# Performance work log

Hardware: AMD Instinct MI355X
Metric: run time of the kernel (lower is better)

The kernel has to match this reference:

```python
import jax, jax.numpy as jnp
import numpy as np

EPS_F = 1e-12
M, N = 64, 4096  # feature dim m, num nodes n


def setup_inputs() -> dict:
    key = jax.random.key(0)
    k1, k2, k3, k4 = jax.random.split(key, 4)
    # X: (m, n) node features transposed, as in the repo (features.t())
    X = jax.random.normal(k1, (M, N), dtype=jnp.float32)
    # F: (m, m) parameter, xavier_uniform init
    bound = float(np.sqrt(6.0 / (M + M)))
    F = jax.random.uniform(k2, (M, M), minval=-bound, maxval=bound, dtype=jnp.float32)
    # Q_S: (n, n) orthogonal eigenvector matrix of the (symmetric, normalized) adjacency
    A = jax.random.normal(k3, (N, N), dtype=jnp.float32)
    Q_S, _ = jnp.linalg.qr(A)
    Q_S = Q_S.astype(jnp.float32)
    # Lambda_S: (n, 1) eigenvalues of normalized adjacency, inside (-1, 1)
    Lambda_S = jnp.sort(
        jax.random.uniform(k4, (N, 1), minval=-0.95, maxval=0.95, dtype=jnp.float32), axis=0
    )
    gamma = jnp.asarray(0.8, dtype=jnp.float32)
    return {"X": X, "F": F, "Q_S": Q_S, "Lambda_S": Lambda_S, "gamma": gamma}


def reference(X, F, Q_S, Lambda_S, gamma):
    # g(F) = F^T F / (||F^T F||_F + eps)  -- Frobenius-normalized Gram matrix
    FF = F.T @ F                                   # (m, m)
    G_F = FF / (jnp.linalg.norm(FF) + EPS_F)       # (m, m), symmetric PSD, ||.||_F ~ 1
    # spectral decomposition of g(F)
    Lambda_F, Q_F = jnp.linalg.eigh(G_F)           # (m,), (m, m)
    # closed-form equilibrium of Z = gamma * g(F) Z S^T + X in the joint eigenbasis
    D = 1.0 / (1.0 - gamma * Lambda_F[:, None] * Lambda_S.reshape(1, -1))  # (m, n)
    Z = Q_F @ (D * (Q_F.T @ X @ Q_S)) @ Q_S.T      # (m, n)
    return Z
```

## Files before the change

kernel.cpp:

```cpp
#include <hip/hip_runtime.h>
#include <math.h>


typedef short short8 __attribute__((ext_vector_type(8)));
typedef float floatx16 __attribute__((ext_vector_type(16)));

#define KSPLIT 16
#define KCHUNK 256
constexpr int Mdim = 64;
constexpr int Ndim = 4096;
constexpr int SLAB = Mdim * Ndim;

__device__ inline ushort f2bf(float f) {
    uint u = __float_as_uint(f);
    u += 0x7fff + ((u >> 16) & 1);
    return (ushort)(u >> 16);
}
__device__ inline float bf2f(ushort h) { return __uint_as_float(((uint)h) << 16); }

__device__ inline floatx16 mfma_bf16(short8 a, short8 b, floatx16 c) {
    return __builtin_amdgcn_mfma_f32_32x32x16_bf16(a, b, c, 0, 0, 0);
}

struct SharedGemm { ushort Ah[4096], Al[4096], Bh[4096], Bl[4096]; };
struct SharedPrep { float Fraw[64 * 65]; ushort Ph[4096], Pl[4096]; float red[256]; };
union SharedU { SharedGemm g; SharedPrep p; };

__device__ void prep_body(SharedPrep& sp, const float* __restrict__ F, float* __restrict__ Gout) {
    const int t = threadIdx.x;
    const int l = t & 63, w = t >> 6;
    const int tm = w & 1, tn = w >> 1;
    const int am = tm * 32 + (l & 31);
    const int bn = tn * 32 + (l & 31);
    const int lk = l >> 5;

    for (int s = 0; s < 4; ++s) {
        int e = t + 256 * s;
        int r = e >> 4, q = (e & 15) * 4;
        float4 v = *(const float4*)&F[r * 64 + q];
        float fa[4] = {v.x, v.y, v.z, v.w};
        for (int i = 0; i < 4; ++i) sp.Fraw[r * 65 + q + i] = fa[i];
    }
    __syncthreads();
    {
        int c = t >> 2, kbase = (t & 3) * 16;
        ushort hh[16], ll[16];
#pragma unroll
        for (int kk = 0; kk < 16; ++kk) {
            float v = sp.Fraw[(kbase + kk) * 65 + c];
            ushort h = f2bf(v);
            hh[kk] = h;
            ll[kk] = f2bf(v - bf2f(h));
        }
#pragma unroll
        for (int g = 0; g < 2; ++g) {
            int gk = (kbase >> 3) + g;
            int idx = c * 64 + ((gk ^ (c & 7)) * 8);
#pragma unroll
            for (int u = 0; u < 8; ++u) { sp.Ph[idx + u] = hh[8 * g + u]; sp.Pl[idx + u] = ll[8 * g + u]; }
        }
    }
    __syncthreads();
    floatx16 acc;
    for (int i = 0; i < 16; ++i) acc[i] = 0.f;
    for (int s16 = 0; s16 < 4; ++s16) {
        int gk = 2 * s16 + lk;
        int ai = am * 64 + ((gk ^ (am & 7)) * 8);
        int bi = bn * 64 + ((gk ^ (bn & 7)) * 8);
        short8 ah = *(const short8*)&sp.Ph[ai];
        short8 al = *(const short8*)&sp.Pl[ai];
        short8 bh = *(const short8*)&sp.Ph[bi];
        short8 bl = *(const short8*)&sp.Pl[bi];
        acc = mfma_bf16(ah, bh, acc);
        acc = mfma_bf16(al, bh, acc);
        acc = mfma_bf16(ah, bl, acc);
    }
    float ss = 0.f;
    for (int r = 0; r < 16; ++r) ss += acc[r] * acc[r];
    sp.red[t] = ss;
    __syncthreads();
    for (int off = 128; off > 0; off >>= 1) {
        if (t < off) sp.red[t] += sp.red[t + off];
        __syncthreads();
    }
    const float inv = 1.0f / (sqrtf(sp.red[0]) + 1e-12f);
    for (int r = 0; r < 16; ++r) {
        int row = (r & 3) + 8 * (r >> 2) + 4 * lk + tm * 32;
        int col = tn * 32 + (l & 31);
        float v = acc[r] * inv;
        Gout[row * 64 + col] = v;
        ushort h = f2bf(v);
        int idx = row * 64 + (((col >> 3) ^ (row & 7)) * 8 + (col & 7));
        sp.Ph[idx] = h;
        sp.Pl[idx] = f2bf(v - bf2f(h));
    }
    for (int j = 1; j < 5; ++j) {
        __syncthreads();
        floatx16 a2;
        for (int i = 0; i < 16; ++i) a2[i] = 0.f;
        for (int s16 = 0; s16 < 4; ++s16) {
            int gk = 2 * s16 + lk;
            int ai = am * 64 + ((gk ^ (am & 7)) * 8);
            int bi = bn * 64 + ((gk ^ (bn & 7)) * 8);
            short8 ah = *(const short8*)&sp.Ph[ai];
            short8 al = *(const short8*)&sp.Pl[ai];
            short8 bh = *(const short8*)&sp.Ph[bi];
            short8 bl = *(const short8*)&sp.Pl[bi];
            a2 = mfma_bf16(ah, bh, a2);
            a2 = mfma_bf16(al, bh, a2);
            a2 = mfma_bf16(ah, bl, a2);
        }
        __syncthreads();
        for (int r = 0; r < 16; ++r) {
            int row = (r & 3) + 8 * (r >> 2) + 4 * lk + tm * 32;
            int col = tn * 32 + (l & 31);
            float v = a2[r];
            Gout[j * 4096 + row * 64 + col] = v;
            ushort h = f2bf(v);
            int idx = row * 64 + (((col >> 3) ^ (row & 7)) * 8 + (col & 7));
            sp.Ph[idx] = h;
            sp.Pl[idx] = f2bf(v - bf2f(h));
        }
    }
}

template <bool TB, bool DOPREP>
__global__ __launch_bounds__(256, 4) void gemm_kernel(const float* __restrict__ A,
                                                      const float* __restrict__ Bm,
                                                      float* __restrict__ C,
                                                      const float* __restrict__ F,
                                                      float* __restrict__ Gp) {
    __shared__ SharedU sh;
    const int bid = blockIdx.x;
    if (DOPREP) {
        if (bid == 0) { prep_body(sh.p, F, Gp); return; }
    }
    const int b = DOPREP ? bid - 1 : bid;
    const int n0 = (b & 63) * 64;
    const int kb = (b >> 6) * KCHUNK;
    const int t = threadIdx.x;
    const int l = t & 63, w = t >> 6;
    const int tm = w & 1, tn = w >> 1;
    const int am = tm * 32 + (l & 31);
    const int bn = tn * 32 + (l & 31);
    const int lk = l >> 5;
    const int sr = t >> 2, sj = t & 3;
    const int nq = t & 15, kr2 = 2 * (t >> 4);

    floatx16 acc;
    for (int i = 0; i < 16; ++i) acc[i] = 0.f;

    for (int step = 0; step < KCHUNK / 64; ++step) {
        const int k0 = kb + step * 64;
        float4 av[4], bv[4], bva[2], bvb[2];
        for (int s = 0; s < 4; ++s)
            av[s] = *(const float4*)&A[sr * 4096 + k0 + 4 * sj + 16 * s];
        if (TB) {
            for (int s = 0; s < 4; ++s)
                bv[s] = *(const float4*)&Bm[(size_t)(n0 + sr) * 4096 + k0 + 4 * sj + 16 * s];
        } else {
            for (int s = 0; s < 2; ++s) {
                bva[s] = *(const float4*)&Bm[(size_t)(k0 + kr2 + 32 * s) * 4096 + n0 + 4 * nq];
                bvb[s] = *(const float4*)&Bm[(size_t)(k0 + kr2 + 1 + 32 * s) * 4096 + n0 + 4 * nq];
            }
        }
        __syncthreads();
        for (int s = 0; s < 4; ++s) {
            int off = 4 * sj + 16 * s;
            int idx = sr * 64 + (((off >> 3) ^ (sr & 7)) * 8 + (off & 7));
            float fa[4] = {av[s].x, av[s].y, av[s].z, av[s].w};
            ushort4 h4, l4;
            ushort* hp = (ushort*)&h4; ushort* lp = (ushort*)&l4;
            for (int i = 0; i < 4; ++i) {
                ushort h = f2bf(fa[i]);
                hp[i] = h; lp[i] = f2bf(fa[i] - bf2f(h));
            }
            *(ushort4*)&sh.g.Ah[idx] = h4;
            *(ushort4*)&sh.g.Al[idx] = l4;
        }
        if (TB) {
            for (int s = 0; s < 4; ++s) {
                int off = 4 * sj + 16 * s;
                int idx = sr * 64 + (((off >> 3) ^ (sr & 7)) * 8 + (off & 7));
                float fb[4] = {bv[s].x, bv[s].y, bv[s].z, bv[s].w};
                ushort4 h4, l4;
                ushort* hp = (ushort*)&h4; ushort* lp = (ushort*)&l4;
                for (int i = 0; i < 4; ++i) {
                    ushort h = f2bf(fb[i]);
                    hp[i] = h; lp[i] = f2bf(fb[i] - bf2f(h));
                }
                *(ushort4*)&sh.g.Bh[idx] = h4;
                *(ushort4*)&sh.g.Bl[idx] = l4;
            }
        } else {
            for (int s = 0; s < 2; ++s) {
                int k = kr2 + 32 * s;
                float fa[4] = {bva[s].x, bva[s].y, bva[s].z, bva[s].w};
                float fb[4] = {bvb[s].x, bvb[s].y, bvb[s].z, bvb[s].w};
                for (int i = 0; i < 4; ++i) {
                    int n = 4 * nq + i;
                    int idx = n * 64 + (((k >> 3) ^ (n & 7)) * 8 + (k & 7));
                    ushort2 hp2, lp2;
                    hp2.x = f2bf(fa[i]); hp2.y = f2bf(fb[i]);
                    lp2.x = f2bf(fa[i] - bf2f(hp2.x));
                    lp2.y = f2bf(fb[i] - bf2f(hp2.y));
                    *(ushort2*)&sh.g.Bh[idx] = hp2;
                    *(ushort2*)&sh.g.Bl[idx] = lp2;
                }
            }
        }
        __syncthreads();
#pragma unroll
        for (int s16 = 0; s16 < 4; ++s16) {
            int gk = 2 * s16 + lk;
            int ai = am * 64 + ((gk ^ (am & 7)) * 8);
            int bi = bn * 64 + ((gk ^ (bn & 7)) * 8);
            short8 ah = *(const short8*)&sh.g.Ah[ai];
            short8 al = *(const short8*)&sh.g.Al[ai];
            short8 bh = *(const short8*)&sh.g.Bh[bi];
            short8 bl = *(const short8*)&sh.g.Bl[bi];
            acc = mfma_bf16(ah, bh, acc);
            acc = mfma_bf16(al, bh, acc);
            acc = mfma_bf16(ah, bl, acc);
        }
    }
    float* Cslab = C + (size_t)(b >> 6) * SLAB;
    const int colg = n0 + tn * 32 + (l & 31);
#pragma unroll
    for (int r = 0; r < 16; ++r) {
        int row = (r & 3) + 8 * (r >> 2) + 4 * lk + tm * 32;
        Cslab[row * 4096 + colg] = acc[r];
    }
}

__global__ __launch_bounds__(256) void solve_kernel(const float* __restrict__ W,
                                                    const float* __restrict__ Gp,
                                                    const float* __restrict__ lam,
                                                    const float* __restrict__ gammap,
                                                    float* __restrict__ Y) {
    __shared__ float Gs[64][68];
    __shared__ float T[64][17];
    const int t = threadIdx.x;
    const int c0 = blockIdx.x * 16;
    for (int e = t; e < 1024; e += 256) {
        const int r = e >> 4, c = c0 + (e & 15);
        float s = 0.f;
#pragma unroll
        for (int bsl = 0; bsl < KSPLIT; ++bsl) s += W[bsl * SLAB + r * 4096 + c];
        T[r][e & 15] = s;
    }
    const int tx = t & 15;
    const int r4 = (t >> 4) * 4;
    const float a = gammap[0] * lam[c0 + tx];
    float s = a;
    for (int j = 0; j < 5; ++j) {
        __syncthreads();
        for (int e = t; e < 4096; e += 256) Gs[e >> 6][e & 63] = Gp[j * 4096 + e];
        __syncthreads();
        float u0 = 0.f, u1 = 0.f, u2 = 0.f, u3 = 0.f;
#pragma unroll 8
        for (int k = 0; k < 64; ++k) {
            const float tv = T[k][tx];
            const float4 g = *(const float4*)&Gs[k][r4];
            u0 += g.x * tv; u1 += g.y * tv; u2 += g.z * tv; u3 += g.w * tv;
        }
        __syncthreads();
        T[r4 + 0][tx] += s * u0;
        T[r4 + 1][tx] += s * u1;
        T[r4 + 2][tx] += s * u2;
        T[r4 + 3][tx] += s * u3;
        s = s * s;
    }
    __syncthreads();
    for (int e = t; e < 1024; e += 256)
        Y[(e >> 4) * 4096 + c0 + (e & 15)] = T[e >> 4][e & 15];
}

__global__ __launch_bounds__(256) void reduce_kernel(const float* __restrict__ P,
                                                     float* __restrict__ Z) {
    const int i = blockIdx.x * 256 + threadIdx.x;
    float4 a = {0.f, 0.f, 0.f, 0.f};
#pragma unroll
    for (int bsl = 0; bsl < KSPLIT; ++bsl) {
        float4 v = *(const float4*)&P[(size_t)bsl * SLAB + i * 4];
        a.x += v.x; a.y += v.y; a.z += v.z; a.w += v.w;
    }
    *(float4*)&Z[i * 4] = a;
}

extern "C" void kernel_launch(void* const* d_in, const int* in_sizes, int n_in,
                              void* d_out, int out_size, void* d_ws, size_t ws_size,
                              hipStream_t stream) {
    const float* X     = (const float*)d_in[0];
    const float* F     = (const float*)d_in[1];
    const float* Qs    = (const float*)d_in[2];
    const float* lam   = (const float*)d_in[3];
    const float* gamma = (const float*)d_in[4];
    float* Z = (float*)d_out;

    float* P1 = (float*)d_ws;
    float* P2 = P1 + (size_t)KSPLIT * SLAB;
    float* Gp = P2 + (size_t)KSPLIT * SLAB;
    float* Y  = Gp + 5 * 4096;

    gemm_kernel<false, true><<<64 * KSPLIT + 1, 256, 0, stream>>>(X, Qs, P1, F, Gp);
    solve_kernel<<<Ndim / 16, 256, 0, stream>>>(P1, Gp, lam, gamma, Y);
    gemm_kernel<true, false><<<64 * KSPLIT, 256, 0, stream>>>(Y, Qs, P2, nullptr, nullptr);
    reduce_kernel<<<256, 256, 0, stream>>>(P2, Z);
}
```

Baseline: 170.3 us.

## Replace split-K partial slabs with atomic accumulation and halve split factor

The split-K GEMMs now accumulate directly into a single output with float atomicAdd instead of writing per-split slabs that later get summed. This removes the separate reduce kernel and the slab summation in the solve kernel. The split factor drops from 16 to 8 with larger K chunks, and a zero-init kernel is added. It cuts workspace traffic and one launch, at the cost of atomic contention, nondeterministic summation order and fewer blocks.

```diff
diff --git a/kernel.cpp b/kernel.cpp
--- a/kernel.cpp
+++ b/kernel.cpp
@@ -5,11 +5,10 @@
 typedef short short8 __attribute__((ext_vector_type(8)));
 typedef float floatx16 __attribute__((ext_vector_type(16)));
 
-#define KSPLIT 16
-#define KCHUNK 256
+#define KSPLIT 8
+#define KCHUNK 512
 constexpr int Mdim = 64;
 constexpr int Ndim = 4096;
-constexpr int SLAB = Mdim * Ndim;
 
 __device__ inline ushort f2bf(float f) {
     uint u = __float_as_uint(f);
@@ -25,6 +24,13 @@
 struct SharedGemm { ushort Ah[4096], Al[4096], Bh[4096], Bl[4096]; };
 struct SharedPrep { float Fraw[64 * 65]; ushort Ph[4096], Pl[4096]; float red[256]; };
 union SharedU { SharedGemm g; SharedPrep p; };
+
+__global__ __launch_bounds__(256) void init_kernel(float* __restrict__ W, float* __restrict__ Z) {
+    const int i = blockIdx.x * 256 + threadIdx.x;
+    float4 z = {0.f, 0.f, 0.f, 0.f};
+    if (i < 65536) *(float4*)&W[i * 4] = z;
+    else *(float4*)&Z[(i - 65536) * 4] = z;
+}
 
 __device__ void prep_body(SharedPrep& sp, const float* __restrict__ F, float* __restrict__ Gout) {
     const int t = threadIdx.x;
@@ -224,12 +230,11 @@
             acc = mfma_bf16(ah, bl, acc);
         }
     }
-    float* Cslab = C + (size_t)(b >> 6) * SLAB;
     const int colg = n0 + tn * 32 + (l & 31);
 #pragma unroll
     for (int r = 0; r < 16; ++r) {
         int row = (r & 3) + 8 * (r >> 2) + 4 * lk + tm * 32;
-        Cslab[row * 4096 + colg] = acc[r];
+        atomicAdd(&C[row * 4096 + colg], acc[r]);
     }
 }
 
@@ -242,13 +247,8 @@
     __shared__ float T[64][17];
     const int t = threadIdx.x;
     const int c0 = blockIdx.x * 16;
-    for (int e = t; e < 1024; e += 256) {
-        const int r = e >> 4, c = c0 + (e & 15);
-        float s = 0.f;
-#pragma unroll
-        for (int bsl = 0; bsl < KSPLIT; ++bsl) s += W[bsl * SLAB + r * 4096 + c];
-        T[r][e & 15] = s;
-    }
+    for (int e = t; e < 1024; e += 256)
+        T[e >> 4][e & 15] = W[(e >> 4) * 4096 + c0 + (e & 15)];
     const int tx = t & 15;
     const int r4 = (t >> 4) * 4;
     const float a = gammap[0] * lam[c0 + tx];
@@ -274,18 +274,6 @@
     __syncthreads();
     for (int e = t; e < 1024; e += 256)
         Y[(e >> 4) * 4096 + c0 + (e & 15)] = T[e >> 4][e & 15];
-}
-
-__global__ __launch_bounds__(256) void reduce_kernel(const float* __restrict__ P,
-                                                     float* __restrict__ Z) {
-    const int i = blockIdx.x * 256 + threadIdx.x;
-    float4 a = {0.f, 0.f, 0.f, 0.f};
-#pragma unroll
-    for (int bsl = 0; bsl < KSPLIT; ++bsl) {
-        float4 v = *(const float4*)&P[(size_t)bsl * SLAB + i * 4];
-        a.x += v.x; a.y += v.y; a.z += v.z; a.w += v.w;
-    }
-    *(float4*)&Z[i * 4] = a;
 }
 
 extern "C" void kernel_launch(void* const* d_in, const int* in_sizes, int n_in,
@@ -298,13 +286,12 @@
     const float* gamma = (const float*)d_in[4];
     float* Z = (float*)d_out;
 
-    float* P1 = (float*)d_ws;
-    float* P2 = P1 + (size_t)KSPLIT * SLAB;
-    float* Gp = P2 + (size_t)KSPLIT * SLAB;
-    float* Y  = Gp + 5 * 4096;
-
-    gemm_kernel<false, true><<<64 * KSPLIT + 1, 256, 0, stream>>>(X, Qs, P1, F, Gp);
-    solve_kernel<<<Ndim / 16, 256, 0, stream>>>(P1, Gp, lam, gamma, Y);
-    gemm_kernel<true, false><<<64 * KSPLIT, 256, 0, stream>>>(Y, Qs, P2, nullptr, nullptr);
-    reduce_kernel<<<256, 256, 0, stream>>>(P2, Z);
-}
+    float* W  = (float*)d_ws;
+    float* Y  = W + Mdim * Ndim;
+    float* Gp = Y + Mdim * Ndim;
+
+    init_kernel<<<512, 256, 0, stream>>>(W, Z);
+    gemm_kernel<false, true><<<64 * KSPLIT + 1, 256, 0, stream>>>(X, Qs, W, F, Gp);
+    solve_kernel<<<Ndim / 16, 256, 0, stream>>>(W, Gp, lam, gamma, Y);
+    gemm_kernel<true, false><<<64 * KSPLIT, 256, 0, stream>>>(Y, Qs, Z, nullptr, nullptr);
+}
```

After: 169.2 us. No clear change (-0.6%).
